# Kernel tuning notes

Measured on AMD Instinct MI355X. Metric: run time of the kernel, lower is better.

Reference implementation:

```python
import jax, jax.numpy as jnp
import numpy as np

NH = 16  # num_attention_heads
DH = 64  # attention_head_size
HS = 1024
LN_EPS = 1e-5


def _linear(x, W, b):
    return jnp.einsum('bsh,oh->bso', x, W) + b


def _mha(q, k, v, mask):
    # q:[B,Sq,H] k,v:[B,Sk,H] mask:[B,Sk] int (1=keep,0=mask)
    B, Sq, _ = q.shape
    Sk = k.shape[1]
    qh = q.reshape(B, Sq, NH, DH).transpose(0, 2, 1, 3)
    kh = k.reshape(B, Sk, NH, DH).transpose(0, 2, 1, 3)
    vh = v.reshape(B, Sk, NH, DH).transpose(0, 2, 1, 3)
    scores = jnp.einsum('bhqd,bhkd->bhqk', qh, kh) / np.sqrt(DH).astype(np.float32)
    if mask is not None:
        scores = jnp.where(mask[:, None, None, :] == 0, jnp.float32(-1e9), scores)
    probs = jax.nn.softmax(scores, axis=-1)  # dropout is identity in eval
    ctx = jnp.einsum('bhqk,bhkd->bhqd', probs, vh)
    return ctx.transpose(0, 2, 1, 3).reshape(B, Sq, NH * DH)


def _layernorm(x, g, b):
    mu = jnp.mean(x, axis=-1, keepdims=True)
    var = jnp.mean(jnp.square(x - mu), axis=-1, keepdims=True)
    return (x - mu) * jax.lax.rsqrt(var + LN_EPS) * g + b


def setup_inputs() -> dict:
    key = jax.random.key(0)
    ks = jax.random.split(key, 20)
    B, Sc, Se = 4, 512, 2048
    s = 0.02
    inp = {
        'claim_embeddings': jax.random.normal(ks[0], (B, Sc, HS), jnp.float32),
        'evidence_embeddings': jax.random.normal(ks[1], (B, Se, HS), jnp.float32),
        'claim_mask': jax.random.randint(ks[2], (B, Sc), 0, 2, jnp.int32),
        'evidence_mask': jax.random.randint(ks[3], (B, Se), 0, 2, jnp.int32),
    }
    names = ['cq', 'ek', 'ev', 'eq', 'ck', 'cv']
    for i, n in enumerate(names):
        inp['W_' + n] = jax.random.normal(ks[4 + i], (HS, HS), jnp.float32) * s
        inp['b_' + n] = jnp.zeros((HS,), jnp.float32)
    inp['ln_g'] = jnp.ones((HS,), jnp.float32)
    inp['ln_b'] = jnp.zeros((HS,), jnp.float32)
    return inp


def reference(claim_embeddings, evidence_embeddings, claim_mask, evidence_mask,
              W_cq, b_cq, W_ek, b_ek, W_ev, b_ev,
              W_eq, b_eq, W_ck, b_ck, W_cv, b_cv, ln_g, ln_b):
    claim_att = _mha(_linear(claim_embeddings, W_cq, b_cq),
                     _linear(evidence_embeddings, W_ek, b_ek),
                     _linear(evidence_embeddings, W_ev, b_ev), evidence_mask)
    evid_att = _mha(_linear(evidence_embeddings, W_eq, b_eq),
                    _linear(claim_embeddings, W_ck, b_ck),
                    _linear(claim_embeddings, W_cv, b_cv), claim_mask)
    claim_out = _layernorm(claim_embeddings + claim_att, ln_g, ln_b)
    evid_out = _layernorm(evidence_embeddings + evid_att, ln_g, ln_b)
    return (claim_out, evid_out)
```

## Files before the change

kernel.cpp:

```cpp
#include <hip/hip_runtime.h>
#include <hip/hip_bf16.h>
#include <stdint.h>
#include <math.h>

typedef __hip_bfloat16 bf16;
typedef __attribute__((ext_vector_type(8))) short bf16x8;
typedef __attribute__((ext_vector_type(4))) float f32x4;

#define DEV __device__ __forceinline__

DEV float lo_bf(unsigned int v) { union { unsigned int u; float f; } c; c.u = v << 16; return c.f; }
DEV float hi_bf(unsigned int v) { union { unsigned int u; float f; } c; c.u = v & 0xffff0000u; return c.f; }
DEV float bs2f(short h) { union { unsigned int u; float f; } c; c.u = ((unsigned int)(unsigned short)h) << 16; return c.f; }

DEV int probe_bf16(const void* ln_g) { return ((const uint16_t*)ln_g)[0] == 0x3F80; }

DEV unsigned short f2bs(float f) { union { bf16 h; unsigned short s; } u; u.h = __float2bfloat16(f); return u.s; }

DEV float ldf(const void* p, size_t i, int bfm) {
    return bfm ? __bfloat162float(((const bf16*)p)[i]) : ((const float*)p)[i];
}

DEV bf16x8 pack8(float4 x, float4 y) {
    union { unsigned short s[8]; bf16x8 v; } u;
    u.s[0] = f2bs(x.x); u.s[1] = f2bs(x.y); u.s[2] = f2bs(x.z); u.s[3] = f2bs(x.w);
    u.s[4] = f2bs(y.x); u.s[5] = f2bs(y.y); u.s[6] = f2bs(y.z); u.s[7] = f2bs(y.w);
    return u.v;
}

DEV bf16x8 ld8cvt(const void* p, size_t i, int bfm) {
    if (bfm) return *(const bf16x8*)((const bf16*)p + i);
    const float4* f = (const float4*)((const float*)p + i);
    return pack8(f[0], f[1]);
}

DEV void gload_lds16(const bf16* g, bf16* l) {
    __builtin_amdgcn_global_load_lds(
        (const __attribute__((address_space(1))) void*)g,
        (__attribute__((address_space(3))) void*)l,
        16, 0, 0);
}

__global__ __launch_bounds__(256) void conv_bf16(
    const void* __restrict__ Xc, const void* __restrict__ Xe,
    const void* __restrict__ W0, const void* __restrict__ W1, const void* __restrict__ W2,
    const void* __restrict__ W3, const void* __restrict__ W4, const void* __restrict__ W5,
    bf16* __restrict__ dst, const void* __restrict__ probe)
{
    const int bfm = probe_bf16(probe);
    const size_t tot = (size_t)16384 * 1024;
    const size_t step = (size_t)gridDim.x * 256 * 8;
    for (size_t e = ((size_t)blockIdx.x * 256 + threadIdx.x) * 8; e < tot; e += step) {
        const size_t row = e >> 10;
        const void* src; size_t off;
        if (row < 2048)       { src = Xc; off = e; }
        else if (row < 10240) { src = Xe; off = e - (size_t)2048 * 1024; }
        else {
            const int wi = (int)((row - 10240) >> 10);
            src = (wi == 0) ? W0 : (wi == 1) ? W1 : (wi == 2) ? W2 :
                  (wi == 3) ? W3 : (wi == 4) ? W4 : W5;
            off = e - (size_t)(10240 + wi * 1024) * 1024;
        }
        *(bf16x8*)(dst + e) = ld8cvt(src, off, bfm);
    }
}

__global__ __launch_bounds__(256) void gemm_fast(
    const bf16* __restrict__ AW,
    const void* __restrict__ B0, const void* __restrict__ B1, const void* __restrict__ B2,
    const void* __restrict__ B3, const void* __restrict__ B4, const void* __restrict__ B5,
    bf16* __restrict__ Out, const void* __restrict__ probe)
{
    __shared__ __align__(16) bf16 As[2][128 * 32];
    __shared__ __align__(16) bf16 Bs[2][128 * 32];

    const int bfm = probe_bf16(probe);
    const int L = (blockIdx.x & 7) * 240 + (blockIdx.x >> 3);
    const int z  = L / 640;
    const int rem = L % 640;
    const int bx = rem >> 3;
    const int by = rem & 7;
    const int rowBase = bx * 128;
    const int colBase = by * 128;
    const int ev = rowBase >= 2048;
    const int widx = z * 2 + ev;

    const bf16* Ap = AW;
    const bf16* Wp = AW + (size_t)(10240 + widx * 1024) * 1024;
    const void* bias = (widx == 0) ? B0 : (widx == 1) ? B1 : (widx == 2) ? B2 :
                       (widx == 3) ? B3 : (widx == 4) ? B4 : B5;
    bf16* O = Out + (size_t)z * 10240 * 1024;

    const int tid  = threadIdx.x;
    const int wave = tid >> 6;
    const int lane = tid & 63;
    const int wm   = wave >> 1;
    const int wn   = wave & 1;
    const int quad = lane >> 4;
    const int l16  = lane & 15;

    f32x4 acc[4][4];
#pragma unroll
    for (int i = 0; i < 4; i++)
#pragma unroll
        for (int j = 0; j < 4; j++) acc[i][j] = (f32x4){0.f, 0.f, 0.f, 0.f};

    const int sr = tid >> 2;
    const int sc = (tid & 3) * 8;
    const size_t ga = (size_t)(rowBase + sr) * 1024 + sc;
    const size_t gb = (size_t)(colBase + sr) * 1024 + sc;

    auto stage = [&](int buf, int k0) {
        gload_lds16(Ap + ga + k0,                     &As[buf][tid * 8]);
        gload_lds16(Ap + ga + (size_t)64 * 1024 + k0, &As[buf][2048 + tid * 8]);
        gload_lds16(Wp + gb + k0,                     &Bs[buf][tid * 8]);
        gload_lds16(Wp + gb + (size_t)64 * 1024 + k0, &Bs[buf][2048 + tid * 8]);
    };

    stage(0, 0);
    __syncthreads();

    int cur = 0;
    for (int k0 = 0; k0 < 1024; k0 += 32) {
        if (k0 + 32 < 1024) stage(cur ^ 1, k0 + 32);

        bf16x8 af[4], bfr[4];
#pragma unroll
        for (int i = 0; i < 4; i++) {
            af[i]  = *(const bf16x8*)(&As[cur][(wm * 64 + i * 16 + l16) * 32 + quad * 8]);
            bfr[i] = *(const bf16x8*)(&Bs[cur][(wn * 64 + i * 16 + l16) * 32 + quad * 8]);
        }
#pragma unroll
        for (int i = 0; i < 4; i++)
#pragma unroll
            for (int j = 0; j < 4; j++)
                acc[i][j] = __builtin_amdgcn_mfma_f32_16x16x32_bf16(af[i], bfr[j], acc[i][j], 0, 0, 0);

        __syncthreads();
        cur ^= 1;
    }

    bf16* Cme = (wn == 0) ? &As[0][0] : &Bs[0][0];
#pragma unroll
    for (int j = 0; j < 4; j++) {
        const int c64 = j * 16 + l16;
        const float bv = ldf(bias, colBase + wn * 64 + c64, bfm);
#pragma unroll
        for (int i = 0; i < 4; i++) {
            const int row0 = wm * 64 + i * 16 + quad * 4;
#pragma unroll
            for (int rr = 0; rr < 4; rr++)
                Cme[(row0 + rr) * 64 + c64] = __float2bfloat16(acc[i][j][rr] + bv);
        }
    }
    __syncthreads();
    const int srow = tid >> 3;
    const int seg  = tid & 7;
#pragma unroll
    for (int pass = 0; pass < 4; pass++) {
        const int row = pass * 32 + srow;
        const bf16x8 v0 = *(const bf16x8*)(&As[0][0] + row * 64 + seg * 8);
        const bf16x8 v1 = *(const bf16x8*)(&Bs[0][0] + row * 64 + seg * 8);
        bf16* orow = O + (size_t)(rowBase + row) * 1024 + colBase;
        *(bf16x8*)(orow + seg * 8)      = v0;
        *(bf16x8*)(orow + 64 + seg * 8) = v1;
    }
}

DEV void attn_core(const bf16* __restrict__ Q, const bf16* __restrict__ K,
                   const bf16* __restrict__ V, const int* __restrict__ mask,
                   bf16* __restrict__ O, int Sk, int h, int qRow0)
{
    __shared__ __align__(16) short Ks [64 * 72];
    __shared__ __align__(16) short VTs[64 * 72];
    __shared__ __align__(16) short Ps [4][16 * 72];

    const int tid  = threadIdx.x;
    const int w    = tid >> 6;
    const int lane = tid & 63;
    const int quad = lane >> 4;
    const int l16  = lane & 15;
    const int qRow = qRow0 + w * 16 + l16;

    const short* Qp = (const short*)Q + (size_t)qRow * 1024 + h * 64;
    const bf16x8 qf0 = *(const bf16x8*)(Qp + quad * 8);
    const bf16x8 qf1 = *(const bf16x8*)(Qp + 32 + quad * 8);

    bf16x8 ones8;
#pragma unroll
    for (int i = 0; i < 8; i++) ones8[i] = (short)0x3F80;

    f32x4 oacc[4];
#pragma unroll
    for (int dt = 0; dt < 4; dt++) oacc[dt] = (f32x4){0.f, 0.f, 0.f, 0.f};
    f32x4 lacc = (f32x4){0.f, 0.f, 0.f, 0.f};

    const int sn = tid >> 2, sseg = tid & 3;
    const int vn2 = (tid & 31) * 2;
    const int vdg = tid >> 5;

    bf16x8 pk0, pk1, pv0, pv1;
    auto loadkv = [&](int k0) {
        const short* src = (const short*)K + (size_t)(k0 + sn) * 1024 + h * 64 + sseg * 16;
        pk0 = *(const bf16x8*)src;
        pk1 = *(const bf16x8*)(src + 8);
        const short* vsrc = (const short*)V + (size_t)(k0 + vn2) * 1024 + h * 64 + vdg * 8;
        pv0 = *(const bf16x8*)vsrc;
        pv1 = *(const bf16x8*)(vsrc + 1024);
    };
    loadkv(0);

    const float SCL = 0.18033688f;
    const float MC  = 1.44269504f;

    for (int k0 = 0; k0 < Sk; k0 += 64) {
        __syncthreads();
        *(bf16x8*)(Ks + sn * 72 + sseg * 16)     = pk0;
        *(bf16x8*)(Ks + sn * 72 + sseg * 16 + 8) = pk1;
#pragma unroll
        for (int i = 0; i < 8; i++) {
            const unsigned int pr = (unsigned short)pv0[i] |
                                    ((unsigned int)(unsigned short)pv1[i] << 16);
            *(unsigned int*)(VTs + (vdg * 8 + i) * 72 + vn2) = pr;
        }
        __syncthreads();
        {
            int kn = k0 + 64; if (kn >= Sk) kn = 0;
            loadkv(kn);
        }

        const int mv_all = mask[k0 + lane];

#pragma unroll
        for (int t = 0; t < 4; t++) {
            const bf16x8 kf0 = *(const bf16x8*)(Ks + (t * 16 + l16) * 72 + quad * 8);
            const bf16x8 kf1 = *(const bf16x8*)(Ks + (t * 16 + l16) * 72 + 32 + quad * 8);
            const float mb = __shfl(mv_all, t * 16 + l16) ? 0.f : -1e9f;
            f32x4 s = (f32x4){mb, mb, mb, mb};
            s = __builtin_amdgcn_mfma_f32_16x16x32_bf16(qf0, kf0, s, 0, 0, 0);
            s = __builtin_amdgcn_mfma_f32_16x16x32_bf16(qf1, kf1, s, 0, 0, 0);
#pragma unroll
            for (int r = 0; r < 4; r++) {
                const float p = __builtin_amdgcn_exp2f(fmaf(s[r], SCL, -MC));
                Ps[w][(quad * 4 + r) * 72 + t * 16 + l16] = f2bs(p);
            }
        }


        const bf16x8 pa0 = *(const bf16x8*)(Ps[w] + l16 * 72 + quad * 8);
        const bf16x8 pa1 = *(const bf16x8*)(Ps[w] + l16 * 72 + 32 + quad * 8);
        lacc = __builtin_amdgcn_mfma_f32_16x16x32_bf16(pa0, ones8, lacc, 0, 0, 0);
        lacc = __builtin_amdgcn_mfma_f32_16x16x32_bf16(pa1, ones8, lacc, 0, 0, 0);
#pragma unroll
        for (int dt = 0; dt < 4; dt++) {
            const bf16x8 vb0 = *(const bf16x8*)(VTs + (dt * 16 + l16) * 72 + quad * 8);
            const bf16x8 vb1 = *(const bf16x8*)(VTs + (dt * 16 + l16) * 72 + 32 + quad * 8);
            oacc[dt] = __builtin_amdgcn_mfma_f32_16x16x32_bf16(pa0, vb0, oacc[dt], 0, 0, 0);
            oacc[dt] = __builtin_amdgcn_mfma_f32_16x16x32_bf16(pa1, vb1, oacc[dt], 0, 0, 0);
        }
    }

    __syncthreads();
#pragma unroll
    for (int r = 0; r < 4; r++) {
        const float inv = 1.0f / fmaxf(lacc[r], 1e-30f);
        const int orow = w * 16 + quad * 4 + r;
#pragma unroll
        for (int dt = 0; dt < 4; dt++)
            Ks[orow * 72 + dt * 16 + l16] = (short)f2bs(oacc[dt][r] * inv);
    }
    __syncthreads();
    const int srow = tid >> 3;
    const int seg  = tid & 7;
    short* Op = (short*)O;
#pragma unroll
    for (int pass = 0; pass < 2; pass++) {
        const int row = pass * 32 + srow;
        const bf16x8 v = *(const bf16x8*)(Ks + row * 72 + seg * 8);
        *(bf16x8*)(Op + (size_t)(qRow0 + row) * 1024 + h * 64 + seg * 8) = v;
    }
}

__global__ __launch_bounds__(256) void attn_flat(
    const bf16* __restrict__ Q1, const bf16* __restrict__ K1, const bf16* __restrict__ V1,
    const int* __restrict__ m1, bf16* __restrict__ O1,
    const bf16* __restrict__ Q2, const bf16* __restrict__ K2, const bf16* __restrict__ V2,
    const int* __restrict__ m2, bf16* __restrict__ O2)
{
    const int xcd = blockIdx.x & 7;
    const int idx = blockIdx.x >> 3;
    const int grp = idx / 5;
    const int pos = idx % 5;

    if (pos == 0) {
        const int j = xcd * 64 + grp;
        const int b = j >> 7;
        const int h = (j >> 3) & 15;
        const int qRow0 = (j & 7) * 64;
        attn_core(Q1 + (size_t)b * 512 * 1024,
                  K1 + (size_t)b * 2048 * 1024,
                  V1 + (size_t)b * 2048 * 1024,
                  m1 + (size_t)b * 2048,
                  O1 + (size_t)b * 512 * 1024, 2048, h, qRow0);
    } else {
        const int j = xcd * 256 + grp * 4 + (pos - 1);
        const int b = j >> 9;
        const int h = (j >> 5) & 15;
        const int qRow0 = (j & 31) * 64;
        attn_core(Q2 + (size_t)b * 2048 * 1024,
                  K2 + (size_t)b * 512 * 1024,
                  V2 + (size_t)b * 512 * 1024,
                  m2 + (size_t)b * 512,
                  O2 + (size_t)b * 2048 * 1024, 512, h, qRow0);
    }
}

__global__ __launch_bounds__(256) void attn_dual(
    const bf16* __restrict__ Q1, const bf16* __restrict__ K1, const bf16* __restrict__ V1,
    const int* __restrict__ m1, bf16* __restrict__ O1,
    const bf16* __restrict__ Q2, const bf16* __restrict__ K2, const bf16* __restrict__ V2,
    const int* __restrict__ m2, bf16* __restrict__ O2)
{
    const int z = blockIdx.z;
    if (z < 4) {
        if (blockIdx.x >= 8) return;
        attn_core(Q1 + (size_t)z * 512 * 1024,
                  K1 + (size_t)z * 2048 * 1024,
                  V1 + (size_t)z * 2048 * 1024,
                  m1 + (size_t)z * 2048,
                  O1 + (size_t)z * 512 * 1024, 2048, blockIdx.y, blockIdx.x * 64);
    } else {
        const int b = z - 4;
        attn_core(Q2 + (size_t)b * 2048 * 1024,
                  K2 + (size_t)b * 512 * 1024,
                  V2 + (size_t)b * 512 * 1024,
                  m2 + (size_t)b * 512,
                  O2 + (size_t)b * 2048 * 1024, 512, blockIdx.y, blockIdx.x * 64);
    }
}

DEV void gemm_core(const void* __restrict__ A, int aRow0,
                   const void* __restrict__ W, const void* __restrict__ bias,
                   bf16* __restrict__ O, int bfm)
{
    __shared__ __align__(16) short As [128 * 40];
    __shared__ __align__(16) short Bsh[128 * 40];

    const int tid  = threadIdx.x;
    const int wave = tid >> 6;
    const int lane = tid & 63;
    const int wm   = wave >> 1;
    const int wn   = wave & 1;
    const int quad = lane >> 4;
    const int l16  = lane & 15;

    const int rowBase = blockIdx.x * 128;
    const int colBase = blockIdx.y * 128;

    f32x4 acc[4][4];
#pragma unroll
    for (int i = 0; i < 4; i++)
#pragma unroll
        for (int j = 0; j < 4; j++) acc[i][j] = (f32x4){0.f, 0.f, 0.f, 0.f};

    const int r  = tid >> 2;
    const int c8 = (tid & 3) * 8;
    const size_t aIdx = (size_t)(aRow0 + rowBase + r) * 1024 + c8;
    const size_t wIdx = (size_t)(colBase + r) * 1024 + c8;
    short* sA0 = As  + r * 40 + c8;
    short* sA1 = As  + (r + 64) * 40 + c8;
    short* sB0 = Bsh + r * 40 + c8;
    short* sB1 = Bsh + (r + 64) * 40 + c8;

    auto compute = [&]() {
        bf16x8 af[4], bfr[4];
#pragma unroll
        for (int i = 0; i < 4; i++) {
            af[i]  = *(const bf16x8*)(As  + (wm * 64 + i * 16 + l16) * 40 + quad * 8);
            bfr[i] = *(const bf16x8*)(Bsh + (wn * 64 + i * 16 + l16) * 40 + quad * 8);
        }
#pragma unroll
        for (int i = 0; i < 4; i++)
#pragma unroll
            for (int j = 0; j < 4; j++)
                acc[i][j] = __builtin_amdgcn_mfma_f32_16x16x32_bf16(af[i], bfr[j], acc[i][j], 0, 0, 0);
    };

    if (bfm) {
        const bf16* Ab = (const bf16*)A;
        const bf16* Wb = (const bf16*)W;
        bf16x8 ra0 = *(const bf16x8*)(Ab + aIdx);
        bf16x8 ra1 = *(const bf16x8*)(Ab + aIdx + (size_t)64 * 1024);
        bf16x8 rb0 = *(const bf16x8*)(Wb + wIdx);
        bf16x8 rb1 = *(const bf16x8*)(Wb + wIdx + (size_t)64 * 1024);
        for (int k0 = 0; k0 < 1024; k0 += 32) {
            __syncthreads();
            *(bf16x8*)sA0 = ra0; *(bf16x8*)sA1 = ra1;
            *(bf16x8*)sB0 = rb0; *(bf16x8*)sB1 = rb1;
            __syncthreads();
            const int kn = (k0 + 32) & 1023;
            ra0 = *(const bf16x8*)(Ab + aIdx + kn);
            ra1 = *(const bf16x8*)(Ab + aIdx + (size_t)64 * 1024 + kn);
            rb0 = *(const bf16x8*)(Wb + wIdx + kn);
            rb1 = *(const bf16x8*)(Wb + wIdx + (size_t)64 * 1024 + kn);
            compute();
        }
    } else {
        const float* Af = (const float*)A;
        const float* Wf = (const float*)W;
        float4 f[4][2];
        auto loadf = [&](int k) {
            f[0][0] = *(const float4*)(Af + aIdx + k);
            f[0][1] = *(const float4*)(Af + aIdx + k + 4);
            f[1][0] = *(const float4*)(Af + aIdx + (size_t)64 * 1024 + k);
            f[1][1] = *(const float4*)(Af + aIdx + (size_t)64 * 1024 + k + 4);
            f[2][0] = *(const float4*)(Wf + wIdx + k);
            f[2][1] = *(const float4*)(Wf + wIdx + k + 4);
            f[3][0] = *(const float4*)(Wf + wIdx + (size_t)64 * 1024 + k);
            f[3][1] = *(const float4*)(Wf + wIdx + (size_t)64 * 1024 + k + 4);
        };
        loadf(0);
        for (int k0 = 0; k0 < 1024; k0 += 32) {
            const bf16x8 ra0 = pack8(f[0][0], f[0][1]);
            const bf16x8 ra1 = pack8(f[1][0], f[1][1]);
            const bf16x8 rb0 = pack8(f[2][0], f[2][1]);
            const bf16x8 rb1 = pack8(f[3][0], f[3][1]);
            __syncthreads();
            *(bf16x8*)sA0 = ra0; *(bf16x8*)sA1 = ra1;
            *(bf16x8*)sB0 = rb0; *(bf16x8*)sB1 = rb1;
            __syncthreads();
            loadf((k0 + 32) & 1023);
            compute();
        }
    }

#pragma unroll
    for (int j = 0; j < 4; j++) {
        const int col = colBase + wn * 64 + j * 16 + l16;
        const float bv = ldf(bias, col, bfm);
#pragma unroll
        for (int i = 0; i < 4; i++) {
            const int row0 = rowBase + wm * 64 + i * 16 + quad * 4;
#pragma unroll
            for (int rr = 0; rr < 4; rr++)
                O[(size_t)(row0 + rr) * 1024 + col] = __float2bfloat16(acc[i][j][rr] + bv);
        }
    }
}

__global__ __launch_bounds__(256) void gemm_bt6(
    const void* __restrict__ Ac, const void* __restrict__ Ae,
    const void* __restrict__ W0, const void* __restrict__ W1, const void* __restrict__ W2,
    const void* __restrict__ W3, const void* __restrict__ W4, const void* __restrict__ W5,
    const void* __restrict__ B0, const void* __restrict__ B1, const void* __restrict__ B2,
    const void* __restrict__ B3, const void* __restrict__ B4, const void* __restrict__ B5,
    bf16* __restrict__ O0, bf16* __restrict__ O1, bf16* __restrict__ O2,
    bf16* __restrict__ O3, bf16* __restrict__ O4, bf16* __restrict__ O5,
    const void* __restrict__ dt_probe)
{
    const int z = blockIdx.z;
    if (z < 3 && blockIdx.x >= 16) return;
    const int bfm = probe_bf16(dt_probe);
    const void* A = (z < 3) ? Ac : Ae;
    const void* W    = (z == 0) ? W0 : (z == 1) ? W1 : (z == 2) ? W2 : (z == 3) ? W3 : (z == 4) ? W4 : W5;
    const void* bias = (z == 0) ? B0 : (z == 1) ? B1 : (z == 2) ? B2 : (z == 3) ? B3 : (z == 4) ? B4 : B5;
    bf16* O          = (z == 0) ? O0 : (z == 1) ? O1 : (z == 2) ? O2 : (z == 3) ? O3 : (z == 4) ? O4 : O5;
    gemm_core(A, 0, W, bias, O, bfm);
}

__global__ __launch_bounds__(256) void ln_wave(
    const void* __restrict__ Xc, const void* __restrict__ Xe, const bf16* __restrict__ Att,
    const void* __restrict__ G, const void* __restrict__ Bb, void* __restrict__ O)
{
    const int bfm = probe_bf16(G);
    const int lane = threadIdx.x & 63;
    const size_t row = (size_t)blockIdx.x * 4 + (threadIdx.x >> 6);
    const void* X; size_t xrow;
    if (row < 2048) { X = Xc; xrow = row; }
    else            { X = Xe; xrow = row - 2048; }

    const int e0 = lane * 16;
    float v[16];
    {
        const short* ap = (const short*)Att + row * 1024 + e0;
        const bf16x8 a0 = *(const bf16x8*)ap;
        const bf16x8 a1 = *(const bf16x8*)(ap + 8);
#pragma unroll
        for (int j = 0; j < 8; j++) { v[j] = bs2f(a0[j]); v[8 + j] = bs2f(a1[j]); }
    }
    if (bfm) {
        const short* xp = (const short*)X + xrow * 1024 + e0;
        const bf16x8 x0 = *(const bf16x8*)xp;
        const bf16x8 x1 = *(const bf16x8*)(xp + 8);
#pragma unroll
        for (int j = 0; j < 8; j++) { v[j] += bs2f(x0[j]); v[8 + j] += bs2f(x1[j]); }
    } else {
        const float* xp = (const float*)X + xrow * 1024 + e0;
#pragma unroll
        for (int q = 0; q < 4; q++) {
            const float4 f = *(const float4*)(xp + q * 4);
            v[q * 4 + 0] += f.x; v[q * 4 + 1] += f.y;
            v[q * 4 + 2] += f.z; v[q * 4 + 3] += f.w;
        }
    }

    float s = 0.f, ss = 0.f;
#pragma unroll
    for (int j = 0; j < 16; j++) { s += v[j]; ss += v[j] * v[j]; }
#pragma unroll
    for (int off = 32; off > 0; off >>= 1) {
        s  += __shfl_xor(s,  off);
        ss += __shfl_xor(ss, off);
    }
    const float mu   = s * (1.f / 1024.f);
    const float var  = ss * (1.f / 1024.f) - mu * mu;
    const float rstd = rsqrtf(var + 1e-5f);

    float g[16], bb[16];
    if (bfm) {
        const short* gp = (const short*)G + e0;
        const short* bp = (const short*)Bb + e0;
        const bf16x8 g0 = *(const bf16x8*)gp, g1 = *(const bf16x8*)(gp + 8);
        const bf16x8 b0 = *(const bf16x8*)bp, b1 = *(const bf16x8*)(bp + 8);
#pragma unroll
        for (int j = 0; j < 8; j++) {
            g[j] = bs2f(g0[j]); g[8 + j] = bs2f(g1[j]);
            bb[j] = bs2f(b0[j]); bb[8 + j] = bs2f(b1[j]);
        }
    } else {
        const float* gp = (const float*)G + e0;
        const float* bp = (const float*)Bb + e0;
#pragma unroll
        for (int q = 0; q < 4; q++) {
            const float4 gf = *(const float4*)(gp + q * 4);
            const float4 bf = *(const float4*)(bp + q * 4);
            g[q * 4 + 0] = gf.x; g[q * 4 + 1] = gf.y; g[q * 4 + 2] = gf.z; g[q * 4 + 3] = gf.w;
            bb[q * 4 + 0] = bf.x; bb[q * 4 + 1] = bf.y; bb[q * 4 + 2] = bf.z; bb[q * 4 + 3] = bf.w;
        }
    }

    float o[16];
#pragma unroll
    for (int j = 0; j < 16; j++) o[j] = (v[j] - mu) * rstd * g[j] + bb[j];

    const size_t obase = row * 1024 + e0;
    if (bfm) {
        union { unsigned short sh[16]; uint4 u[2]; } pk;
#pragma unroll
        for (int j = 0; j < 16; j++) pk.sh[j] = f2bs(o[j]);
        uint4* op = (uint4*)((bf16*)O + obase);
        op[0] = pk.u[0]; op[1] = pk.u[1];
    } else {
        float* op = (float*)O + obase;
#pragma unroll
        for (int q = 0; q < 4; q++)
            *(float4*)(op + q * 4) = (float4){o[q * 4], o[q * 4 + 1], o[q * 4 + 2], o[q * 4 + 3]};
    }
}

DEV void ln_body(const void* __restrict__ X, size_t xrow, const bf16* __restrict__ Att,
                 size_t arow, const void* __restrict__ G, const void* __restrict__ Bb,
                 void* __restrict__ O, size_t orow, int bfm)
{
    __shared__ float r1[4], r2[4];
    const int tid = threadIdx.x;
    const size_t abase = arow * 1024 + tid * 4;
    const size_t xbase = xrow * 1024 + tid * 4;
    const uint2 ab = *(const uint2*)(Att + abase);
    const float v0 = ldf(X, xbase + 0, bfm) + lo_bf(ab.x);
    const float v1 = ldf(X, xbase + 1, bfm) + hi_bf(ab.x);
    const float v2 = ldf(X, xbase + 2, bfm) + lo_bf(ab.y);
    const float v3 = ldf(X, xbase + 3, bfm) + hi_bf(ab.y);
    float s  = v0 + v1 + v2 + v3;
    float ss = v0 * v0 + v1 * v1 + v2 * v2 + v3 * v3;
    for (int off = 32; off > 0; off >>= 1) { s += __shfl_down(s, off); ss += __shfl_down(ss, off); }
    if ((tid & 63) == 0) { r1[tid >> 6] = s; r2[tid >> 6] = ss; }
    __syncthreads();
    const float S  = r1[0] + r1[1] + r1[2] + r1[3];
    const float SS = r2[0] + r2[1] + r2[2] + r2[3];
    const float mu   = S * (1.f / 1024.f);
    const float var  = SS * (1.f / 1024.f) - mu * mu;
    const float rstd = rsqrtf(var + 1e-5f);
    const float g0 = ldf(G, tid * 4 + 0, bfm), g1 = ldf(G, tid * 4 + 1, bfm);
    const float g2 = ldf(G, tid * 4 + 2, bfm), g3 = ldf(G, tid * 4 + 3, bfm);
    const float bb0 = ldf(Bb, tid * 4 + 0, bfm), bb1 = ldf(Bb, tid * 4 + 1, bfm);
    const float bb2 = ldf(Bb, tid * 4 + 2, bfm), bb3 = ldf(Bb, tid * 4 + 3, bfm);
    const float o0 = (v0 - mu) * rstd * g0 + bb0;
    const float o1 = (v1 - mu) * rstd * g1 + bb1;
    const float o2 = (v2 - mu) * rstd * g2 + bb2;
    const float o3 = (v3 - mu) * rstd * g3 + bb3;
    const size_t obase = orow * 1024 + tid * 4;
    if (bfm) {
        union { unsigned short s4[4]; uint2 u; } pack;
        pack.s4[0] = f2bs(o0); pack.s4[1] = f2bs(o1); pack.s4[2] = f2bs(o2); pack.s4[3] = f2bs(o3);
        *(uint2*)((bf16*)O + obase) = pack.u;
    } else {
        *(float4*)((float*)O + obase) = (float4){o0, o1, o2, o3};
    }
}

__global__ __launch_bounds__(256) void ln_kernel(
    const void* __restrict__ X, int xRow0, const bf16* __restrict__ Att,
    const void* __restrict__ G, const void* __restrict__ Bb,
    void* __restrict__ O, size_t oRow0)
{
    const int bfm = probe_bf16(G);
    const size_t row = blockIdx.x;
    ln_body(X, (size_t)xRow0 + row, Att, row, G, Bb, O, oRow0 + row, bfm);
}

extern "C" void kernel_launch(void* const* d_in, const int* in_sizes, int n_in,
                              void* d_out, int out_size, void* d_ws, size_t ws_size,
                              hipStream_t stream)
{
    (void)in_sizes; (void)n_in; (void)out_size;

    const void* c_emb  = d_in[0];
    const void* e_emb  = d_in[1];
    const int*  c_mask = (const int*)d_in[2];
    const int*  e_mask = (const int*)d_in[3];
    const void* W_cq = d_in[4];  const void* b_cq = d_in[5];
    const void* W_ek = d_in[6];  const void* b_ek = d_in[7];
    const void* W_ev = d_in[8];  const void* b_ev = d_in[9];
    const void* W_eq = d_in[10]; const void* b_eq = d_in[11];
    const void* W_ck = d_in[12]; const void* b_ck = d_in[13];
    const void* W_cv = d_in[14]; const void* b_cv = d_in[15];
    const void* ln_g = d_in[16]; const void* ln_b = d_in[17];

    const int B = 4, Scl = 512, Sev = 2048;
    const size_t MC = (size_t)B * Scl;
    const size_t ME = (size_t)B * Sev;
    const size_t MT = MC + ME;
    const size_t RW = MT * 1024;

    dim3 blk(256);
    const size_t need_fast = (3 * RW + (size_t)16384 * 1024) * sizeof(bf16);

    if (ws_size >= need_fast) {
        bf16* Qr = (bf16*)d_ws;
        bf16* Kr = Qr + RW;
        bf16* Vr = Kr + RW;
        bf16* CV = Vr + RW;

        conv_bf16<<<dim3(2048), blk, 0, stream>>>(
            c_emb, e_emb, W_cq, W_eq, W_ck, W_ek, W_cv, W_ev, CV, ln_g);

        gemm_fast<<<dim3(1920), blk, 0, stream>>>(
            CV, b_cq, b_eq, b_ck, b_ek, b_cv, b_ev, Qr, ln_g);

        attn_flat<<<dim3(2560), blk, 0, stream>>>(
            Qr,             Kr + MC * 1024, Vr + MC * 1024, e_mask, Qr,
            Qr + MC * 1024, Kr,             Vr,             c_mask, Qr + MC * 1024);

        ln_wave<<<dim3((unsigned)(MT / 4)), blk, 0, stream>>>(
            c_emb, e_emb, Qr, ln_g, ln_b, d_out);
    } else {
        bf16* q_c = (bf16*)d_ws;
        bf16* k_c = q_c + MC * 1024;
        bf16* v_c = k_c + MC * 1024;
        bf16* q_e = v_c + MC * 1024;
        bf16* k_e = q_e + ME * 1024;
        bf16* v_e = k_e + ME * 1024;

        gemm_bt6<<<dim3(64, 8, 6), blk, 0, stream>>>(
            c_emb, e_emb,
            W_cq, W_ck, W_cv, W_eq, W_ek, W_ev,
            b_cq, b_ck, b_cv, b_eq, b_ek, b_ev,
            q_c, k_c, v_c, q_e, k_e, v_e, ln_g);

        attn_dual<<<dim3(32, 16, 8), blk, 0, stream>>>(
            q_c, k_e, v_e, e_mask, q_c,
            q_e, k_c, v_c, c_mask, q_e);

        ln_kernel<<<dim3((unsigned)MC), blk, 0, stream>>>(
            c_emb, 0, q_c, ln_g, ln_b, d_out, 0);
        ln_kernel<<<dim3((unsigned)ME), blk, 0, stream>>>(
            e_emb, 0, q_e, ln_g, ln_b, d_out, MC);
    }
}
```

Measured before the change: 349.9 us.

## Process 128 query rows per attention block to reuse K/V tiles

Adds attn_core2, where each block handles two 64-row query tiles against every staged K/V tile, so each K/V load from global memory and each LDS transpose is shared by twice as many queries. The next K/V tile is also prefetched into registers while the current one is being computed. The grid is halved and the block-to-work mapping is updated to match. In exchange, register pressure rises from the doubled accumulators, and with fewer blocks the GPU may be less fully occupied.

```diff
diff --git a/kernel.cpp b/kernel.cpp
--- a/kernel.cpp
+++ b/kernel.cpp
@@ -167,6 +167,167 @@
     }
 }
 
+DEV void attn_core2(const bf16* __restrict__ Q, const bf16* __restrict__ K,
+                    const bf16* __restrict__ V, const int* __restrict__ mask,
+                    bf16* __restrict__ O, int Sk, int h, int qRow0)
+{
+    __shared__ __align__(16) short Ks [64 * 72];
+    __shared__ __align__(16) short VTs[64 * 72];
+    __shared__ __align__(16) short Ps [4][16 * 72];
+
+    const int tid  = threadIdx.x;
+    const int w    = tid >> 6;
+    const int lane = tid & 63;
+    const int quad = lane >> 4;
+    const int l16  = lane & 15;
+
+    bf16x8 qf[2][2];
+#pragma unroll
+    for (int mt = 0; mt < 2; mt++) {
+        const short* Qp = (const short*)Q +
+            (size_t)(qRow0 + mt * 64 + w * 16 + l16) * 1024 + h * 64;
+        qf[mt][0] = *(const bf16x8*)(Qp + quad * 8);
+        qf[mt][1] = *(const bf16x8*)(Qp + 32 + quad * 8);
+    }
+
+    bf16x8 ones8;
+#pragma unroll
+    for (int i = 0; i < 8; i++) ones8[i] = (short)0x3F80;
+
+    f32x4 oacc[2][4];
+    f32x4 lacc[2];
+#pragma unroll
+    for (int mt = 0; mt < 2; mt++) {
+        lacc[mt] = (f32x4){0.f, 0.f, 0.f, 0.f};
+#pragma unroll
+        for (int dt = 0; dt < 4; dt++) oacc[mt][dt] = (f32x4){0.f, 0.f, 0.f, 0.f};
+    }
+
+    const int sn = tid >> 2, sseg = tid & 3;
+    const int vn2 = (tid & 31) * 2;
+    const int vdg = tid >> 5;
+
+    bf16x8 pk0, pk1, pv0, pv1;
+    int pm;
+    auto loadkv = [&](int k0) {
+        const short* src = (const short*)K + (size_t)(k0 + sn) * 1024 + h * 64 + sseg * 16;
+        pk0 = *(const bf16x8*)src;
+        pk1 = *(const bf16x8*)(src + 8);
+        const short* vsrc = (const short*)V + (size_t)(k0 + vn2) * 1024 + h * 64 + vdg * 8;
+        pv0 = *(const bf16x8*)vsrc;
+        pv1 = *(const bf16x8*)(vsrc + 1024);
+        pm  = mask[k0 + lane];
+    };
+    loadkv(0);
+
+    const float SCL = 0.18033688f;
+    const float MC  = 1.44269504f;
+
+    for (int k0 = 0; k0 < Sk; k0 += 64) {
+        __syncthreads();
+        *(bf16x8*)(Ks + sn * 72 + sseg * 16)     = pk0;
+        *(bf16x8*)(Ks + sn * 72 + sseg * 16 + 8) = pk1;
+#pragma unroll
+        for (int i = 0; i < 8; i++) {
+            const unsigned int pr = (unsigned short)pv0[i] |
+                                    ((unsigned int)(unsigned short)pv1[i] << 16);
+            *(unsigned int*)(VTs + (vdg * 8 + i) * 72 + vn2) = pr;
+        }
+        __syncthreads();
+        const int mv_all = pm;
+        {
+            int kn = k0 + 64; if (kn >= Sk) kn = 0;
+            loadkv(kn);
+        }
+
+#pragma unroll
+        for (int mt = 0; mt < 2; mt++) {
+#pragma unroll
+            for (int t = 0; t < 4; t++) {
+                const bf16x8 kf0 = *(const bf16x8*)(Ks + (t * 16 + l16) * 72 + quad * 8);
+                const bf16x8 kf1 = *(const bf16x8*)(Ks + (t * 16 + l16) * 72 + 32 + quad * 8);
+                const float mb = __shfl(mv_all, t * 16 + l16) ? 0.f : -1e9f;
+                f32x4 s = (f32x4){mb, mb, mb, mb};
+                s = __builtin_amdgcn_mfma_f32_16x16x32_bf16(qf[mt][0], kf0, s, 0, 0, 0);
+                s = __builtin_amdgcn_mfma_f32_16x16x32_bf16(qf[mt][1], kf1, s, 0, 0, 0);
+#pragma unroll
+                for (int r = 0; r < 4; r++) {
+                    const float p = __builtin_amdgcn_exp2f(fmaf(s[r], SCL, -MC));
+                    Ps[w][(quad * 4 + r) * 72 + t * 16 + l16] = f2bs(p);
+                }
+            }
+            const bf16x8 pa0 = *(const bf16x8*)(Ps[w] + l16 * 72 + quad * 8);
+            const bf16x8 pa1 = *(const bf16x8*)(Ps[w] + l16 * 72 + 32 + quad * 8);
+            lacc[mt] = __builtin_amdgcn_mfma_f32_16x16x32_bf16(pa0, ones8, lacc[mt], 0, 0, 0);
+            lacc[mt] = __builtin_amdgcn_mfma_f32_16x16x32_bf16(pa1, ones8, lacc[mt], 0, 0, 0);
+#pragma unroll
+            for (int dt = 0; dt < 4; dt++) {
+                const bf16x8 vb0 = *(const bf16x8*)(VTs + (dt * 16 + l16) * 72 + quad * 8);
+                const bf16x8 vb1 = *(const bf16x8*)(VTs + (dt * 16 + l16) * 72 + 32 + quad * 8);
+                oacc[mt][dt] = __builtin_amdgcn_mfma_f32_16x16x32_bf16(pa0, vb0, oacc[mt][dt], 0, 0, 0);
+                oacc[mt][dt] = __builtin_amdgcn_mfma_f32_16x16x32_bf16(pa1, vb1, oacc[mt][dt], 0, 0, 0);
+            }
+        }
+    }
+
+    const int srow = tid >> 3;
+    const int seg  = tid & 7;
+    short* Op = (short*)O;
+#pragma unroll
+    for (int mt = 0; mt < 2; mt++) {
+        __syncthreads();
+#pragma unroll
+        for (int r = 0; r < 4; r++) {
+            const float inv = 1.0f / fmaxf(lacc[mt][r], 1e-30f);
+            const int orow = w * 16 + quad * 4 + r;
+#pragma unroll
+            for (int dt = 0; dt < 4; dt++)
+                Ks[orow * 72 + dt * 16 + l16] = (short)f2bs(oacc[mt][dt][r] * inv);
+        }
+        __syncthreads();
+#pragma unroll
+        for (int pass = 0; pass < 2; pass++) {
+            const int row = pass * 32 + srow;
+            const bf16x8 v = *(const bf16x8*)(Ks + row * 72 + seg * 8);
+            *(bf16x8*)(Op + (size_t)(qRow0 + mt * 64 + row) * 1024 + h * 64 + seg * 8) = v;
+        }
+    }
+}
+
+__global__ __launch_bounds__(256) void attn_flat(
+    const bf16* __restrict__ Q1, const bf16* __restrict__ K1, const bf16* __restrict__ V1,
+    const int* __restrict__ m1, bf16* __restrict__ O1,
+    const bf16* __restrict__ Q2, const bf16* __restrict__ K2, const bf16* __restrict__ V2,
+    const int* __restrict__ m2, bf16* __restrict__ O2)
+{
+    const int xcd = blockIdx.x & 7;
+    const int idx = blockIdx.x >> 3;
+    const int grp = idx / 5;
+    const int pos = idx % 5;
+
+    if (pos == 0) {
+        const int j = xcd * 32 + grp;
+        const int b = j >> 6;
+        const int h = (j >> 2) & 15;
+        const int qRow0 = (j & 3) * 128;
+        attn_core2(Q1 + (size_t)b * 512 * 1024,
+                   K1 + (size_t)b * 2048 * 1024,
+                   V1 + (size_t)b * 2048 * 1024,
+                   m1 + (size_t)b * 2048,
+                   O1 + (size_t)b * 512 * 1024, 2048, h, qRow0);
+    } else {
+        const int j = xcd * 128 + grp * 4 + (pos - 1);
+        const int b = j >> 8;
+        const int h = (j >> 4) & 15;
+        const int qRow0 = (j & 15) * 128;
+        attn_core2(Q2 + (size_t)b * 2048 * 1024,
+                   K2 + (size_t)b * 512 * 1024,
+                   V2 + (size_t)b * 512 * 1024,
+                   m2 + (size_t)b * 512,
+                   O2 + (size_t)b * 2048 * 1024, 512, h, qRow0);
+    }
+}
+
 DEV void attn_core(const bf16* __restrict__ Q, const bf16* __restrict__ K,
                    const bf16* __restrict__ V, const int* __restrict__ mask,
                    bf16* __restrict__ O, int Sk, int h, int qRow0)
@@ -246,7 +407,6 @@
             }
         }
 
-
         const bf16x8 pa0 = *(const bf16x8*)(Ps[w] + l16 * 72 + quad * 8);
         const bf16x8 pa1 = *(const bf16x8*)(Ps[w] + l16 * 72 + 32 + quad * 8);
         lacc = __builtin_amdgcn_mfma_f32_16x16x32_bf16(pa0, ones8, lacc, 0, 0, 0);
@@ -278,40 +438,6 @@
         const int row = pass * 32 + srow;
         const bf16x8 v = *(const bf16x8*)(Ks + row * 72 + seg * 8);
         *(bf16x8*)(Op + (size_t)(qRow0 + row) * 1024 + h * 64 + seg * 8) = v;
-    }
-}
-
-__global__ __launch_bounds__(256) void attn_flat(
-    const bf16* __restrict__ Q1, const bf16* __restrict__ K1, const bf16* __restrict__ V1,
-    const int* __restrict__ m1, bf16* __restrict__ O1,
-    const bf16* __restrict__ Q2, const bf16* __restrict__ K2, const bf16* __restrict__ V2,
-    const int* __restrict__ m2, bf16* __restrict__ O2)
-{
-    const int xcd = blockIdx.x & 7;
-    const int idx = blockIdx.x >> 3;
-    const int grp = idx / 5;
-    const int pos = idx % 5;
-
-    if (pos == 0) {
-        const int j = xcd * 64 + grp;
-        const int b = j >> 7;
-        const int h = (j >> 3) & 15;
-        const int qRow0 = (j & 7) * 64;
-        attn_core(Q1 + (size_t)b * 512 * 1024,
-                  K1 + (size_t)b * 2048 * 1024,
-                  V1 + (size_t)b * 2048 * 1024,
-                  m1 + (size_t)b * 2048,
-                  O1 + (size_t)b * 512 * 1024, 2048, h, qRow0);
-    } else {
-        const int j = xcd * 256 + grp * 4 + (pos - 1);
-        const int b = j >> 9;
-        const int h = (j >> 5) & 15;
-        const int qRow0 = (j & 31) * 64;
-        attn_core(Q2 + (size_t)b * 2048 * 1024,
-                  K2 + (size_t)b * 512 * 1024,
-                  V2 + (size_t)b * 512 * 1024,
-                  m2 + (size_t)b * 512,
-                  O2 + (size_t)b * 2048 * 1024, 512, h, qRow0);
     }
 }
 
@@ -648,7 +774,7 @@
         gemm_fast<<<dim3(1920), blk, 0, stream>>>(
             CV, b_cq, b_eq, b_ck, b_ek, b_cv, b_ev, Qr, ln_g);
 
-        attn_flat<<<dim3(2560), blk, 0, stream>>>(
+        attn_flat<<<dim3(1280), blk, 0, stream>>>(
             Qr,             Kr + MC * 1024, Vr + MC * 1024, e_mask, Qr,
             Qr + MC * 1024, Kr,             Vr,             c_mask, Qr + MC * 1024);
 
```

Measured after the change: 356.8 us. No clear change (+2.0%).
